# Kernel optimization log

Hardware: AMD Instinct MI355X
Metric: run time of the kernel (lower is better)

Reference implementation:

```python
import jax, jax.numpy as jnp
import numpy as np

PATCH = 16
EPS = 1e-5


def _conv_offsets(x, offset_w, offset_b):
    # offset conv: same kernel/stride/padding as the deform conv
    off = jax.lax.conv_general_dilated(
        x, offset_w, window_strides=(PATCH, PATCH), padding='VALID',
        dimension_numbers=('NCHW', 'OIHW', 'NCHW'))
    return off + offset_b[None, :, None, None]


def _deform_conv(x, offset_w, offset_b, dconv_w):
    B, C, H, W = x.shape
    kh = kw = PATCH
    K = kh * kw
    Ho, Wo = H // PATCH, W // PATCH

    off = _conv_offsets(x, offset_w, offset_b)            # [B, 2K, Ho, Wo]
    # mmcv layout: channels are (dy, dx) pairs per kernel point
    off = off.reshape(B, K, 2, Ho, Wo)
    dy = off[:, :, 0].transpose(0, 2, 3, 1)               # [B, Ho, Wo, K]
    dx = off[:, :, 1].transpose(0, 2, 3, 1)

    ii, jj = jnp.meshgrid(jnp.arange(kh), jnp.arange(kw), indexing='ij')
    ki = ii.reshape(-1).astype(x.dtype)                   # [K]
    kj = jj.reshape(-1).astype(x.dtype)
    base_y = (jnp.arange(Ho, dtype=x.dtype) * PATCH)[:, None] + ki[None, :]  # [Ho, K]
    base_x = (jnp.arange(Wo, dtype=x.dtype) * PATCH)[:, None] + kj[None, :]  # [Wo, K]

    py = base_y[None, :, None, :] + dy                    # [B, Ho, Wo, K]
    px = base_x[None, None, :, :] + dx

    y0 = jnp.floor(py); x0 = jnp.floor(px)
    wy1 = py - y0; wx1 = px - x0
    wy0 = 1.0 - wy1; wx0 = 1.0 - wx1
    y0i = y0.astype(jnp.int32); x0i = x0.astype(jnp.int32)
    y1i = y0i + 1;              x1i = x0i + 1

    xt = x.transpose(0, 2, 3, 1)                          # [B, H, W, C]
    bidx = jnp.arange(B)[:, None, None, None]

    def gather(yi, xi):
        ok = ((yi >= 0) & (yi < H) & (xi >= 0) & (xi < W)).astype(x.dtype)
        v = xt[bidx, jnp.clip(yi, 0, H - 1), jnp.clip(xi, 0, W - 1)]  # [B,Ho,Wo,K,C]
        return v * ok[..., None]

    sampled = (gather(y0i, x0i) * (wy0 * wx0)[..., None]
               + gather(y0i, x1i) * (wy0 * wx1)[..., None]
               + gather(y1i, x0i) * (wy1 * wx0)[..., None]
               + gather(y1i, x1i) * (wy1 * wx1)[..., None])  # [B,Ho,Wo,K,C]

    Wk = dconv_w.reshape(dconv_w.shape[0], C, K)          # [O, C, K]
    out = jnp.einsum('bhwkc,ock->bohw', sampled, Wk)      # [B, O, Ho, Wo]
    return out


def setup_inputs() -> dict:
    key = jax.random.key(0)
    ks = jax.random.split(key, 3)
    B, C, H, W = 64, 3, 224, 224
    O = 768
    x = jax.random.normal(ks[0], (B, C, H, W), jnp.float32)
    # small offset weights -> offsets of O(1) pixel, exercising bilinear path
    offset_w = jax.random.normal(ks[1], (2 * PATCH * PATCH, C, PATCH, PATCH), jnp.float32) * 0.01
    offset_b = jnp.zeros((2 * PATCH * PATCH,), jnp.float32)
    dconv_w = jax.random.normal(ks[2], (O, C, PATCH, PATCH), jnp.float32) * 0.02
    bn_gamma = jnp.ones((O,), jnp.float32)
    bn_beta = jnp.zeros((O,), jnp.float32)
    return {"x": x, "offset_w": offset_w, "offset_b": offset_b,
            "dconv_w": dconv_w, "bn_gamma": bn_gamma, "bn_beta": bn_beta}


def reference(x, offset_w, offset_b, dconv_w, bn_gamma, bn_beta):
    B = x.shape[0]
    y = _deform_conv(x, offset_w, offset_b, dconv_w)      # [B, O, Ho, Wo]
    # BatchNorm2d (training-mode batch stats, biased var) per torch semantics
    mean = jnp.mean(y, axis=(0, 2, 3), keepdims=True)
    var = jnp.mean((y - mean) ** 2, axis=(0, 2, 3), keepdims=True)
    yn = (y - mean) * jax.lax.rsqrt(var + EPS)
    yn = yn * bn_gamma[None, :, None, None] + bn_beta[None, :, None, None]
    ya = jax.nn.gelu(yn, approximate=False)               # nn.GELU default = exact
    O, Ho, Wo = ya.shape[1], ya.shape[2], ya.shape[3]
    return ya.reshape(B, O, Ho * Wo).transpose(0, 2, 1)   # [B, N, embed_dim]
```

## Files before the change

### kernel.cpp

```cpp
#include <hip/hip_runtime.h>
#include <math.h>

#define PATCH 16
#define BATCH 64
#define CIN 3
#define HH 224
#define WW 224
#define NPATCH (BATCH*14*14)
#define KDIM 768
#define NOFF 512
#define NOUT 768
#define KPTS 256
#define EPSF 1e-5f
#define CHW (CIN*HH*WW)
#define HWX (HH*WW)
#define NRB (NPATCH/128)

using short8 = __attribute__((ext_vector_type(8))) short;
using f32x4  = __attribute__((ext_vector_type(4))) float;

#define GLOAD16(g, l) __builtin_amdgcn_global_load_lds( \
    (const __attribute__((address_space(1))) void*)(g), \
    (__attribute__((address_space(3))) void*)(l), 16, 0, 0)

__device__ __forceinline__ unsigned short f2bf(float f) {
    unsigned int u = __float_as_uint(f);
    u = (u + 0x7fffu + ((u >> 16) & 1u)) >> 16;
    return (unsigned short)u;
}
__device__ __forceinline__ float bf2f(unsigned short h) {
    return __uint_as_float(((unsigned int)h) << 16);
}
__device__ __forceinline__ float gelu_exact(float v) {
    return 0.5f * v * (1.0f + erff(v * 0.70710678118654752440f));
}

#define N4X (BATCH*CHW/4)
#define N4W1 (NOFF*KDIM/4)
#define N4W2 (NOUT*KDIM/4)
#define N4ALL (N4X+N4W1+N4W2)

__global__ __launch_bounds__(256) void cvt_all(
    const float* __restrict__ x, const float* __restrict__ w1,
    const float* __restrict__ w2, unsigned short* __restrict__ xbf,
    unsigned short* __restrict__ wbf1, unsigned short* __restrict__ wbf2)
{
    for (int i = blockIdx.x*256 + threadIdx.x; i < N4ALL; i += gridDim.x*256) {
        const float* src; unsigned short* dst; int j;
        if (i < N4X)            { src = x;  dst = xbf;  j = i; }
        else if (i < N4X+N4W1)  { src = w1; dst = wbf1; j = i - N4X; }
        else                    { src = w2; dst = wbf2; j = i - N4X - N4W1; }
        float4 v = ((const float4*)src)[j];
        ((ushort4*)dst)[j] = make_ushort4(f2bf(v.x), f2bf(v.y), f2bf(v.z), f2bf(v.w));
    }
}

__global__ __launch_bounds__(256) void gemm_offsets(
    const unsigned short* __restrict__ xbf, const unsigned short* __restrict__ Bw,
    const float* __restrict__ offb, unsigned short* __restrict__ off)
{
    __shared__ unsigned short lds[4*8192];
    const int t = threadIdx.x;
    const int lane = t & 63;
    const int w = t >> 6, wr = w >> 1, wc = w & 1;

    int bid = blockIdx.x;
    int idx = (bid & 7)*49 + (bid >> 3);
    const int bm = (idx >> 2) * 128, bn = (idx & 3) * 128;

    const int rq = t >> 2;
    const int ksw = (((t & 3) ^ ((t >> 3) & 3)) << 3);

    const unsigned short* aBase0;
    const unsigned short* aBase1;
    {
        int p0 = bm + rq,      b0 = p0/196, r0 = p0%196;
        int p1 = bm + 64 + rq, b1 = p1/196, r1 = p1%196;
        aBase0 = xbf + (size_t)b0*CHW + (size_t)((r0/14)*PATCH)*WW + (size_t)((r0%14)*PATCH);
        aBase1 = xbf + (size_t)b1*CHW + (size_t)((r1/14)*PATCH)*WW + (size_t)((r1%14)*PATCH);
    }
    const unsigned short* bS0 = Bw + (size_t)(bn + rq)*KDIM + ksw;
    const unsigned short* bS1 = Bw + (size_t)(bn + 64 + rq)*KDIM + ksw;

    const int row_a = wr*64 + (lane & 15);
    const int row_b = wc*64 + (lane & 15);
    const int klocs = (((lane >> 4) ^ ((lane >> 1) & 3)) << 3);

#define STG1(slot, k0) do { \
        unsigned short* d = lds + (slot)*8192 + t*8; \
        int e = (k0) + ksw; \
        size_t xo = (size_t)(e >> 8)*HWX + (size_t)((e >> 4) & 15)*WW + (e & 15); \
        GLOAD16(aBase0 + xo, d); \
        GLOAD16(aBase1 + xo, d + 2048); \
        GLOAD16(bS0 + (k0), d + 4096); \
        GLOAD16(bS1 + (k0), d + 6144); \
    } while(0)

    f32x4 acc[4][4] = {};
    STG1(0, 0); STG1(1, 32); STG1(2, 64);
    asm volatile("s_waitcnt vmcnt(8)" ::: "memory");
    __builtin_amdgcn_s_barrier();
#pragma unroll
    for (int it = 0; it < 24; ++it) {
        if (it + 3 < 24) STG1((it+3)&3, (it+3)*32);
        const unsigned short* As_ = lds + (it&3)*8192;
        const unsigned short* Bs_ = As_ + 4096;
        short8 af[4], bv[4];
#pragma unroll
        for (int m = 0; m < 4; ++m) af[m] = *(const short8*)&As_[(row_a + m*16)*32 + klocs];
#pragma unroll
        for (int n = 0; n < 4; ++n) bv[n] = *(const short8*)&Bs_[(row_b + n*16)*32 + klocs];
        __builtin_amdgcn_s_setprio(1);
#pragma unroll
        for (int m = 0; m < 4; ++m)
#pragma unroll
            for (int n = 0; n < 4; ++n)
                acc[m][n] = __builtin_amdgcn_mfma_f32_16x16x32_bf16(af[m], bv[n], acc[m][n], 0, 0, 0);
        __builtin_amdgcn_s_setprio(0);
        if (it <= 20)      { asm volatile("s_waitcnt vmcnt(8) lgkmcnt(0)" ::: "memory"); __builtin_amdgcn_s_barrier(); }
        else if (it == 21) { asm volatile("s_waitcnt vmcnt(4) lgkmcnt(0)" ::: "memory"); __builtin_amdgcn_s_barrier(); }
        else if (it == 22) { asm volatile("s_waitcnt vmcnt(0) lgkmcnt(0)" ::: "memory"); __builtin_amdgcn_s_barrier(); }
    }
#undef STG1

    const int col0 = bn + wc*64 + (lane & 15);
    const int r0 = (lane >> 4) * 4;
#pragma unroll
    for (int m = 0; m < 4; ++m) {
        int grow = bm + wr*64 + m*16 + r0;
#pragma unroll
        for (int n = 0; n < 4; ++n) {
            int gcol = col0 + n*16;
            float bias = offb[gcol];
#pragma unroll
            for (int r = 0; r < 4; ++r)
                off[(size_t)(grow + r)*NOFF + gcol] = f2bf(acc[m][n][r] + bias);
        }
    }
}

__global__ __launch_bounds__(256) void sampler(
    const unsigned short* __restrict__ xbf, const unsigned int* __restrict__ offu,
    unsigned short* __restrict__ A2)
{
    __shared__ unsigned short win[3][22][24];
    int p = blockIdx.x;
    int k = threadIdx.x;
    int b = p / 196, rem = p % 196;
    int ho = rem / 14, wo = rem % 14;
    const int gy0 = ho*PATCH - 2, gx0 = wo*PATCH - 2;
    const unsigned short* xb = xbf + (size_t)b*CHW;

    bool interior = (ho >= 1) && (ho <= 12) && (wo >= 1) && (wo <= 12);
    if (interior) {
        for (int idx = k; idx < 3*22*11; idx += 256) {
            int c = idx / 242, r2 = idx - c*242;
            int row = r2 / 11, u = r2 - row*11;
            const unsigned int* src = (const unsigned int*)
                (xb + (size_t)c*HWX + (size_t)(gy0+row)*WW + gx0);
            *(unsigned int*)&win[c][row][2*u] = src[u];
        }
    } else {
        for (int idx = k; idx < 3*22*22; idx += 256) {
            int c = idx / 484, r2 = idx - c*484;
            int row = r2 / 22, col = r2 - row*22;
            int gy = min(max(gy0+row, 0), HH-1);
            int gx = min(max(gx0+col, 0), WW-1);
            win[c][row][col] = xb[(size_t)c*HWX + (size_t)gy*WW + gx];
        }
    }
    __syncthreads();

    unsigned int d2 = offu[(size_t)p*KPTS + k];
    float dy = __uint_as_float((d2 & 0xffffu) << 16);
    float dx = __uint_as_float(d2 & 0xffff0000u);
    float py = (float)(ho*PATCH + (k >> 4)) + dy;
    float px = (float)(wo*PATCH + (k & 15)) + dx;
    float fy = floorf(py), fx = floorf(px);
    float wy1 = py - fy, wx1 = px - fx;
    float wy0 = 1.f - wy1, wx0 = 1.f - wx1;
    int y0 = (int)fy, x0 = (int)fx;
    int y1 = y0 + 1, x1 = x0 + 1;
    bool oky0 = (y0 >= 0) & (y0 < HH);
    bool oky1 = (y1 >= 0) & (y1 < HH);
    bool okx0 = (x0 >= 0) & (x0 < WW);
    bool okx1 = (x1 >= 0) & (x1 < WW);
    float w00 = wy0*wx0, w01 = wy0*wx1, w10 = wy1*wx0, w11 = wy1*wx1;

    int ry = y0 - gy0, rx = x0 - gx0;
    if (ry >= 0 && ry <= 20 && rx >= 0 && rx <= 20) {
        float m00 = oky0 && okx0 ? 1.f : 0.f;
        float m01 = oky0 && okx1 ? 1.f : 0.f;
        float m10 = oky1 && okx0 ? 1.f : 0.f;
        float m11 = oky1 && okx1 ? 1.f : 0.f;
#pragma unroll
        for (int c = 0; c < CIN; ++c) {
            float v00 = bf2f(win[c][ry  ][rx  ]) * m00;
            float v01 = bf2f(win[c][ry  ][rx+1]) * m01;
            float v10 = bf2f(win[c][ry+1][rx  ]) * m10;
            float v11 = bf2f(win[c][ry+1][rx+1]) * m11;
            float v = v00*w00 + v01*w01 + v10*w10 + v11*w11;
            A2[(size_t)p*KDIM + c*KPTS + k] = f2bf(v);
        }
    } else {
        int yc0 = min(max(y0, 0), HH-1), yc1 = min(max(y1, 0), HH-1);
        int xc0 = min(max(x0, 0), WW-1), xc1 = min(max(x1, 0), WW-1);
#pragma unroll
        for (int c = 0; c < CIN; ++c) {
            const unsigned short* xc = xb + (size_t)c*HWX;
            float v00 = (oky0 && okx0) ? bf2f(xc[(size_t)yc0*WW + xc0]) : 0.f;
            float v01 = (oky0 && okx1) ? bf2f(xc[(size_t)yc0*WW + xc1]) : 0.f;
            float v10 = (oky1 && okx0) ? bf2f(xc[(size_t)yc1*WW + xc0]) : 0.f;
            float v11 = (oky1 && okx1) ? bf2f(xc[(size_t)yc1*WW + xc1]) : 0.f;
            float v = v00*w00 + v01*w01 + v10*w10 + v11*w11;
            A2[(size_t)p*KDIM + c*KPTS + k] = f2bf(v);
        }
    }
}

__global__ __launch_bounds__(512) void gemm_deform(
    const unsigned short* __restrict__ A, const unsigned short* __restrict__ Bw,
    unsigned short* __restrict__ Cbf, float* __restrict__ psum, float* __restrict__ psq)
{
    __shared__ unsigned short lds[4*16384];
    const int t = threadIdx.x;
    const int lane = t & 63;
    const int w = t >> 6;
    const int wr = w >> 2, wc = w & 3;

    int bid = blockIdx.x;
    int xcd = bid & 7, jj = bid >> 3;
    int idx = (xcd < 3) ? xcd*19 + jj : 57 + (xcd-3)*18 + jj;
    const int mblk = idx / 3;
    const int bm = mblk*256, bn = (idx % 3)*256;

    const int schunk = ((t & 3) ^ ((t >> 3) & 3)) << 3;
    const unsigned short* aSrc = A  + (size_t)(bm + (t >> 2))*KDIM + schunk;
    const unsigned short* bSrc = Bw + (size_t)(bn + (t >> 2))*KDIM + schunk;

#define STG_A(s, k0) do { \
        unsigned short* d = lds + (s)*16384 + t*8; \
        GLOAD16(aSrc + (k0), d); \
        GLOAD16(aSrc + (size_t)128*KDIM + (k0), d + 4096); } while(0)
#define STG_B(s, k0) do { \
        unsigned short* d = lds + (s)*16384 + 8192 + t*8; \
        GLOAD16(bSrc + (k0), d); \
        GLOAD16(bSrc + (size_t)128*KDIM + (k0), d + 4096); } while(0)

    const int klocs = (((lane >> 4) ^ ((lane >> 1) & 3)) << 3);
    const int arow0 = wr*128 + (lane & 15);
    const int brow0 = wc*64  + (lane & 15);

    f32x4 acc[8][4] = {};

    STG_A(0, 0);  STG_B(0, 0);
    STG_A(1, 32); STG_B(1, 32);
    asm volatile("s_waitcnt vmcnt(4)" ::: "memory");
    __builtin_amdgcn_s_barrier();

    short8 af[8], bv[4];
    for (int kt = 0; kt < 12; ++kt) {
        const int s0 = (2*kt) & 3;
        const int s1 = s0 + 1;
        const int s2 = (s0 + 2) & 3;
        const int s3 = (s0 + 3) & 3;
        const int k2 = (2*kt + 2) * 32;
        const int k3 = (2*kt + 3) * 32;
        const unsigned short* H0 = lds + s0*16384;
        const unsigned short* H1 = lds + s1*16384;

#pragma unroll
        for (int m = 0; m < 8; ++m) af[m] = *(const short8*)&H0[(arow0 + m*16)*32 + klocs];
        bv[0] = *(const short8*)&H0[8192 + (brow0 +  0)*32 + klocs];
        bv[1] = *(const short8*)&H0[8192 + (brow0 + 16)*32 + klocs];
        if (kt < 11) STG_A(s2, k2);
        __builtin_amdgcn_s_barrier();
        asm volatile("s_waitcnt lgkmcnt(0)" ::: "memory");
        __builtin_amdgcn_s_setprio(1);
#pragma unroll
        for (int m = 0; m < 8; ++m) {
            acc[m][0] = __builtin_amdgcn_mfma_f32_16x16x32_bf16(af[m], bv[0], acc[m][0], 0, 0, 0);
            acc[m][1] = __builtin_amdgcn_mfma_f32_16x16x32_bf16(af[m], bv[1], acc[m][1], 0, 0, 0);
        }
        __builtin_amdgcn_s_setprio(0);
        asm volatile("s_waitcnt lgkmcnt(0)" ::: "memory");
        __builtin_amdgcn_s_barrier();

        bv[2] = *(const short8*)&H0[8192 + (brow0 + 32)*32 + klocs];
        bv[3] = *(const short8*)&H0[8192 + (brow0 + 48)*32 + klocs];
        if (kt < 11) { STG_B(s2, k2);
            asm volatile("s_waitcnt vmcnt(4)" ::: "memory");
        } else {
            asm volatile("s_waitcnt vmcnt(0)" ::: "memory");
        }
        __builtin_amdgcn_s_barrier();
        asm volatile("s_waitcnt lgkmcnt(0)" ::: "memory");
        __builtin_amdgcn_s_setprio(1);
#pragma unroll
        for (int m = 0; m < 8; ++m) {
            acc[m][2] = __builtin_amdgcn_mfma_f32_16x16x32_bf16(af[m], bv[2], acc[m][2], 0, 0, 0);
            acc[m][3] = __builtin_amdgcn_mfma_f32_16x16x32_bf16(af[m], bv[3], acc[m][3], 0, 0, 0);
        }
        __builtin_amdgcn_s_setprio(0);
        asm volatile("s_waitcnt lgkmcnt(0)" ::: "memory");
        __builtin_amdgcn_s_barrier();

#pragma unroll
        for (int m = 0; m < 8; ++m) af[m] = *(const short8*)&H1[(arow0 + m*16)*32 + klocs];
        bv[0] = *(const short8*)&H1[8192 + (brow0 +  0)*32 + klocs];
        bv[1] = *(const short8*)&H1[8192 + (brow0 + 16)*32 + klocs];
        if (kt < 11) STG_A(s3, k3);
        __builtin_amdgcn_s_barrier();
        asm volatile("s_waitcnt lgkmcnt(0)" ::: "memory");
        __builtin_amdgcn_s_setprio(1);
#pragma unroll
        for (int m = 0; m < 8; ++m) {
            acc[m][0] = __builtin_amdgcn_mfma_f32_16x16x32_bf16(af[m], bv[0], acc[m][0], 0, 0, 0);
            acc[m][1] = __builtin_amdgcn_mfma_f32_16x16x32_bf16(af[m], bv[1], acc[m][1], 0, 0, 0);
        }
        __builtin_amdgcn_s_setprio(0);
        asm volatile("s_waitcnt lgkmcnt(0)" ::: "memory");
        __builtin_amdgcn_s_barrier();

        bv[2] = *(const short8*)&H1[8192 + (brow0 + 32)*32 + klocs];
        bv[3] = *(const short8*)&H1[8192 + (brow0 + 48)*32 + klocs];
        if (kt < 11) { STG_B(s3, k3);
            asm volatile("s_waitcnt vmcnt(4)" ::: "memory");
        }
        __builtin_amdgcn_s_barrier();
        asm volatile("s_waitcnt lgkmcnt(0)" ::: "memory");
        __builtin_amdgcn_s_setprio(1);
#pragma unroll
        for (int m = 0; m < 8; ++m) {
            acc[m][2] = __builtin_amdgcn_mfma_f32_16x16x32_bf16(af[m], bv[2], acc[m][2], 0, 0, 0);
            acc[m][3] = __builtin_amdgcn_mfma_f32_16x16x32_bf16(af[m], bv[3], acc[m][3], 0, 0, 0);
        }
        __builtin_amdgcn_s_setprio(0);
        asm volatile("s_waitcnt lgkmcnt(0)" ::: "memory");
        __builtin_amdgcn_s_barrier();
    }
#undef STG_A
#undef STG_B

    float s[4] = {}, q[4] = {};
#pragma unroll
    for (int m = 0; m < 8; ++m)
#pragma unroll
        for (int n = 0; n < 4; ++n)
#pragma unroll
            for (int r = 0; r < 4; ++r) {
                float v = acc[m][n][r];
                s[n] += v; q[n] += v*v;
            }
#pragma unroll
    for (int n = 0; n < 4; ++n) {
        s[n] += __shfl_xor(s[n], 16); q[n] += __shfl_xor(q[n], 16);
        s[n] += __shfl_xor(s[n], 32); q[n] += __shfl_xor(q[n], 32);
    }

    __syncthreads();
    float* redS = (float*)lds;
    float* redQ = redS + 512;
    if (lane < 16) {
#pragma unroll
        for (int n = 0; n < 4; ++n) {
            redS[wr*256 + wc*64 + n*16 + lane] = s[n];
            redQ[wr*256 + wc*64 + n*16 + lane] = q[n];
        }
    }
    __syncthreads();

    const int col0 = bn + wc*64 + (lane & 15);
    const int r0 = (lane >> 4) * 4;
#pragma unroll
    for (int m = 0; m < 8; ++m) {
        int grow = bm + wr*128 + m*16 + r0;
#pragma unroll
        for (int n = 0; n < 4; ++n) {
            int gcol = col0 + n*16;
#pragma unroll
            for (int r = 0; r < 4; ++r)
                Cbf[(size_t)(grow + r)*NOUT + gcol] = f2bf(acc[m][n][r]);
        }
    }
    {
        int half = t >> 8;
        int c = t & 255;
        psum[(size_t)(bm/128 + half)*NOUT + bn + c] = redS[half*256 + c];
        psq [(size_t)(bm/128 + half)*NOUT + bn + c] = redQ[half*256 + c];
    }
}

__global__ __launch_bounds__(256) void bn_final(
    const float* __restrict__ psum, const float* __restrict__ psq,
    const float* __restrict__ gamma, const float* __restrict__ beta,
    float* __restrict__ scale, float* __restrict__ shift)
{
    int o = blockIdx.x*256 + threadIdx.x;
    float s = 0.f, q = 0.f;
    for (int i = 0; i < NRB; ++i) {
        s += psum[(size_t)i*NOUT + o];
        q += psq [(size_t)i*NOUT + o];
    }
    float mean = s * (1.0f/(float)NPATCH);
    float var  = q * (1.0f/(float)NPATCH) - mean*mean;
    float inv  = 1.0f / sqrtf(var + EPSF);
    float sc   = gamma[o] * inv;
    scale[o] = sc;
    shift[o] = beta[o] - mean*sc;
}

__global__ __launch_bounds__(256) void norm_gelu(
    const unsigned short* __restrict__ ybf, float* __restrict__ out,
    const float* __restrict__ scale, const float* __restrict__ shift)
{
    __shared__ float ssc[NOUT], ssh[NOUT];
    for (int i = threadIdx.x; i < NOUT; i += 256) { ssc[i] = scale[i]; ssh[i] = shift[i]; }
    __syncthreads();
    const size_t total8 = (size_t)NPATCH * NOUT / 8;
    for (size_t i = (size_t)blockIdx.x*256 + threadIdx.x; i < total8;
         i += (size_t)gridDim.x*256) {
        uint4 v = ((const uint4*)ybf)[i];
        int og = (int)(i % (NOUT/8)) * 8;
        float4 o0, o1;
        o0.x = gelu_exact(__uint_as_float(v.x << 16)        * ssc[og+0] + ssh[og+0]);
        o0.y = gelu_exact(__uint_as_float(v.x & 0xffff0000u)* ssc[og+1] + ssh[og+1]);
        o0.z = gelu_exact(__uint_as_float(v.y << 16)        * ssc[og+2] + ssh[og+2]);
        o0.w = gelu_exact(__uint_as_float(v.y & 0xffff0000u)* ssc[og+3] + ssh[og+3]);
        o1.x = gelu_exact(__uint_as_float(v.z << 16)        * ssc[og+4] + ssh[og+4]);
        o1.y = gelu_exact(__uint_as_float(v.z & 0xffff0000u)* ssc[og+5] + ssh[og+5]);
        o1.z = gelu_exact(__uint_as_float(v.w << 16)        * ssc[og+6] + ssh[og+6]);
        o1.w = gelu_exact(__uint_as_float(v.w & 0xffff0000u)* ssc[og+7] + ssh[og+7]);
        ((float4*)out)[2*i]   = o0;
        ((float4*)out)[2*i+1] = o1;
    }
}

extern "C" void kernel_launch(void* const* d_in, const int* in_sizes, int n_in,
                              void* d_out, int out_size, void* d_ws, size_t ws_size,
                              hipStream_t stream)
{
    const float* x      = (const float*)d_in[0];
    const float* offw   = (const float*)d_in[1];
    const float* offb   = (const float*)d_in[2];
    const float* dconvw = (const float*)d_in[3];
    const float* gamma  = (const float*)d_in[4];
    const float* beta   = (const float*)d_in[5];
    float* out = (float*)d_out;

    const size_t NX  = (size_t)BATCH*CHW;
    const size_t NW1 = (size_t)NOFF*KDIM;
    const size_t NW2 = (size_t)NOUT*KDIM;

    unsigned short* xbf   = (unsigned short*)d_ws;
    unsigned short* wbf1  = xbf  + NX;
    unsigned short* wbf2  = wbf1 + NW1;
    unsigned short* A2    = wbf2 + NW2;
    unsigned short* off   = A2   + (size_t)NPATCH*KDIM;
    unsigned short* ybf   = off  + (size_t)NPATCH*NOFF;
    float* fscratch = (float*)(ybf + (size_t)NPATCH*NOUT);
    float* psum  = fscratch;
    float* psq   = psum + NRB*NOUT;
    float* scale = psq  + NRB*NOUT;
    float* shift = scale + NOUT;

    cvt_all<<<4096, 256, 0, stream>>>(x, offw, dconvw, xbf, wbf1, wbf2);
    gemm_offsets<<<392, 256, 0, stream>>>(xbf, wbf1, offb, off);
    sampler<<<NPATCH, 256, 0, stream>>>(xbf, (const unsigned int*)off, A2);
    gemm_deform<<<147, 512, 0, stream>>>(A2, wbf2, ybf, psum, psq);
    bn_final<<<3, 256, 0, stream>>>(psum, psq, gamma, beta, scale, shift);
    norm_gelu<<<2048, 256, 0, stream>>>(ybf, out, scale, shift);
}
```

Baseline: 102.7 us.

## Drop separate bf16 conversion of input; read fp32 x directly in GEMM and sampler

Removes the bf16 conversion pass over the input image. The offset GEMM now stages fp32 patches into LDS and packs them to bf16 in registers before the MFMA, and the sampler reads fp32 directly. The conversion kernel now only handles the weights. This saves a full read and write of x, at the cost of more LDS per stage (pipeline depth cut from 4 to 3 slots), twice the A-tile global traffic, and truncating rather than rounding the GEMM's A operand to bf16.

Result: slower. 107.5 us (+4.7%).

```diff
diff --git a/kernel.cpp b/kernel.cpp
--- a/kernel.cpp
+++ b/kernel.cpp
@@ -28,38 +28,35 @@
     u = (u + 0x7fffu + ((u >> 16) & 1u)) >> 16;
     return (unsigned short)u;
 }
-__device__ __forceinline__ float bf2f(unsigned short h) {
-    return __uint_as_float(((unsigned int)h) << 16);
-}
 __device__ __forceinline__ float gelu_exact(float v) {
     return 0.5f * v * (1.0f + erff(v * 0.70710678118654752440f));
 }
-
-#define N4X (BATCH*CHW/4)
+__device__ __forceinline__ unsigned int pk2(float lo, float hi) {
+    return (__float_as_uint(hi) & 0xffff0000u) | (__float_as_uint(lo) >> 16);
+}
+
 #define N4W1 (NOFF*KDIM/4)
 #define N4W2 (NOUT*KDIM/4)
-#define N4ALL (N4X+N4W1+N4W2)
-
-__global__ __launch_bounds__(256) void cvt_all(
-    const float* __restrict__ x, const float* __restrict__ w1,
-    const float* __restrict__ w2, unsigned short* __restrict__ xbf,
+#define N4W  (N4W1+N4W2)
+
+__global__ __launch_bounds__(256) void cvt_w(
+    const float* __restrict__ w1, const float* __restrict__ w2,
     unsigned short* __restrict__ wbf1, unsigned short* __restrict__ wbf2)
 {
-    for (int i = blockIdx.x*256 + threadIdx.x; i < N4ALL; i += gridDim.x*256) {
-        const float* src; unsigned short* dst; int j;
-        if (i < N4X)            { src = x;  dst = xbf;  j = i; }
-        else if (i < N4X+N4W1)  { src = w1; dst = wbf1; j = i - N4X; }
-        else                    { src = w2; dst = wbf2; j = i - N4X - N4W1; }
-        float4 v = ((const float4*)src)[j];
-        ((ushort4*)dst)[j] = make_ushort4(f2bf(v.x), f2bf(v.y), f2bf(v.z), f2bf(v.w));
-    }
+    int i = blockIdx.x*256 + threadIdx.x;
+    if (i >= N4W) return;
+    const float* src; unsigned short* dst; int j;
+    if (i < N4W1) { src = w1; dst = wbf1; j = i; }
+    else          { src = w2; dst = wbf2; j = i - N4W1; }
+    float4 v = ((const float4*)src)[j];
+    ((ushort4*)dst)[j] = make_ushort4(f2bf(v.x), f2bf(v.y), f2bf(v.z), f2bf(v.w));
 }
 
 __global__ __launch_bounds__(256) void gemm_offsets(
-    const unsigned short* __restrict__ xbf, const unsigned short* __restrict__ Bw,
+    const float* __restrict__ x, const unsigned short* __restrict__ Bw,
     const float* __restrict__ offb, unsigned short* __restrict__ off)
 {
-    __shared__ unsigned short lds[4*8192];
+    __shared__ unsigned short lds[3*12288];
     const int t = threadIdx.x;
     const int lane = t & 63;
     const int w = t >> 6, wr = w >> 1, wc = w & 1;
@@ -68,48 +65,60 @@
     int idx = (bid & 7)*49 + (bid >> 3);
     const int bm = (idx >> 2) * 128, bn = (idx & 3) * 128;
 
+    const int sccA = (t & 7) ^ ((t >> 3) & 7);
+    const float* aBase[4];
+#pragma unroll
+    for (int o = 0; o < 4; ++o) {
+        int p = bm + o*32 + (t >> 3);
+        int b = p / 196, rem = p % 196;
+        int ho = rem / 14, wo = rem % 14;
+        aBase[o] = x + (size_t)b*CHW + (size_t)(ho*PATCH)*WW + (size_t)(wo*PATCH);
+    }
     const int rq = t >> 2;
-    const int ksw = (((t & 3) ^ ((t >> 3) & 3)) << 3);
-
-    const unsigned short* aBase0;
-    const unsigned short* aBase1;
-    {
-        int p0 = bm + rq,      b0 = p0/196, r0 = p0%196;
-        int p1 = bm + 64 + rq, b1 = p1/196, r1 = p1%196;
-        aBase0 = xbf + (size_t)b0*CHW + (size_t)((r0/14)*PATCH)*WW + (size_t)((r0%14)*PATCH);
-        aBase1 = xbf + (size_t)b1*CHW + (size_t)((r1/14)*PATCH)*WW + (size_t)((r1%14)*PATCH);
-    }
-    const unsigned short* bS0 = Bw + (size_t)(bn + rq)*KDIM + ksw;
-    const unsigned short* bS1 = Bw + (size_t)(bn + 64 + rq)*KDIM + ksw;
+    const int kswB = (((t & 3) ^ ((t >> 3) & 3)) << 3);
+    const unsigned short* bS0 = Bw + (size_t)(bn + rq)*KDIM + kswB;
+    const unsigned short* bS1 = Bw + (size_t)(bn + 64 + rq)*KDIM + kswB;
 
     const int row_a = wr*64 + (lane & 15);
     const int row_b = wc*64 + (lane & 15);
-    const int klocs = (((lane >> 4) ^ ((lane >> 1) & 3)) << 3);
+    const int cA0 = ((lane >> 4) << 1) ^ (lane & 7);
+    const int klocsB = (((lane >> 4) ^ ((lane >> 1) & 3)) << 3);
 
 #define STG1(slot, k0) do { \
-        unsigned short* d = lds + (slot)*8192 + t*8; \
-        int e = (k0) + ksw; \
+        unsigned short* dA = lds + (slot)*12288 + t*8; \
+        int e = (k0) + sccA*4; \
         size_t xo = (size_t)(e >> 8)*HWX + (size_t)((e >> 4) & 15)*WW + (e & 15); \
-        GLOAD16(aBase0 + xo, d); \
-        GLOAD16(aBase1 + xo, d + 2048); \
-        GLOAD16(bS0 + (k0), d + 4096); \
-        GLOAD16(bS1 + (k0), d + 6144); \
+        GLOAD16(aBase[0] + xo, dA); \
+        GLOAD16(aBase[1] + xo, dA + 2048); \
+        GLOAD16(aBase[2] + xo, dA + 4096); \
+        GLOAD16(aBase[3] + xo, dA + 6144); \
+        unsigned short* dB = lds + (slot)*12288 + 8192 + t*8; \
+        GLOAD16(bS0 + (k0), dB); \
+        GLOAD16(bS1 + (k0), dB + 2048); \
     } while(0)
 
     f32x4 acc[4][4] = {};
-    STG1(0, 0); STG1(1, 32); STG1(2, 64);
-    asm volatile("s_waitcnt vmcnt(8)" ::: "memory");
+    STG1(0, 0); STG1(1, 32);
+    asm volatile("s_waitcnt vmcnt(6)" ::: "memory");
     __builtin_amdgcn_s_barrier();
 #pragma unroll
     for (int it = 0; it < 24; ++it) {
-        if (it + 3 < 24) STG1((it+3)&3, (it+3)*32);
-        const unsigned short* As_ = lds + (it&3)*8192;
-        const unsigned short* Bs_ = As_ + 4096;
+        if (it + 2 < 24) STG1((it+2)%3, (it+2)*32);
+        const float* Af = (const float*)(lds + (it%3)*12288);
+        const unsigned short* Bs_ = lds + (it%3)*12288 + 8192;
         short8 af[4], bv[4];
 #pragma unroll
-        for (int m = 0; m < 4; ++m) af[m] = *(const short8*)&As_[(row_a + m*16)*32 + klocs];
-#pragma unroll
-        for (int n = 0; n < 4; ++n) bv[n] = *(const short8*)&Bs_[(row_b + n*16)*32 + klocs];
+        for (int m = 0; m < 4; ++m) {
+            int rb = (row_a + m*16)*32;
+            f32x4 v0 = *(const f32x4*)&Af[rb + cA0*4];
+            f32x4 v1 = *(const f32x4*)&Af[rb + (cA0^1)*4];
+            uint4 u;
+            u.x = pk2(v0[0], v0[1]); u.y = pk2(v0[2], v0[3]);
+            u.z = pk2(v1[0], v1[1]); u.w = pk2(v1[2], v1[3]);
+            af[m] = *(short8*)&u;
+        }
+#pragma unroll
+        for (int n = 0; n < 4; ++n) bv[n] = *(const short8*)&Bs_[(row_b + n*16)*32 + klocsB];
         __builtin_amdgcn_s_setprio(1);
 #pragma unroll
         for (int m = 0; m < 4; ++m)
@@ -117,8 +126,7 @@
             for (int n = 0; n < 4; ++n)
                 acc[m][n] = __builtin_amdgcn_mfma_f32_16x16x32_bf16(af[m], bv[n], acc[m][n], 0, 0, 0);
         __builtin_amdgcn_s_setprio(0);
-        if (it <= 20)      { asm volatile("s_waitcnt vmcnt(8) lgkmcnt(0)" ::: "memory"); __builtin_amdgcn_s_barrier(); }
-        else if (it == 21) { asm volatile("s_waitcnt vmcnt(4) lgkmcnt(0)" ::: "memory"); __builtin_amdgcn_s_barrier(); }
+        if (it < 22)       { asm volatile("s_waitcnt vmcnt(6) lgkmcnt(0)" ::: "memory"); __builtin_amdgcn_s_barrier(); }
         else if (it == 22) { asm volatile("s_waitcnt vmcnt(0) lgkmcnt(0)" ::: "memory"); __builtin_amdgcn_s_barrier(); }
     }
 #undef STG1
@@ -140,25 +148,24 @@
 }
 
 __global__ __launch_bounds__(256) void sampler(
-    const unsigned short* __restrict__ xbf, const unsigned int* __restrict__ offu,
+    const float* __restrict__ x, const unsigned int* __restrict__ offu,
     unsigned short* __restrict__ A2)
 {
-    __shared__ unsigned short win[3][22][24];
+    __shared__ float win[3][22][24];
     int p = blockIdx.x;
     int k = threadIdx.x;
     int b = p / 196, rem = p % 196;
     int ho = rem / 14, wo = rem % 14;
     const int gy0 = ho*PATCH - 2, gx0 = wo*PATCH - 2;
-    const unsigned short* xb = xbf + (size_t)b*CHW;
+    const float* xb = x + (size_t)b*CHW;
 
     bool interior = (ho >= 1) && (ho <= 12) && (wo >= 1) && (wo <= 12);
     if (interior) {
         for (int idx = k; idx < 3*22*11; idx += 256) {
             int c = idx / 242, r2 = idx - c*242;
             int row = r2 / 11, u = r2 - row*11;
-            const unsigned int* src = (const unsigned int*)
-                (xb + (size_t)c*HWX + (size_t)(gy0+row)*WW + gx0);
-            *(unsigned int*)&win[c][row][2*u] = src[u];
+            float2 s = *(const float2*)(xb + (size_t)c*HWX + (size_t)(gy0+row)*WW + gx0 + 2*u);
+            *(float2*)&win[c][row][2*u] = s;
         }
     } else {
         for (int idx = k; idx < 3*22*22; idx += 256) {
@@ -195,11 +202,10 @@
         float m11 = oky1 && okx1 ? 1.f : 0.f;
 #pragma unroll
         for (int c = 0; c < CIN; ++c) {
-            float v00 = bf2f(win[c][ry  ][rx  ]) * m00;
-            float v01 = bf2f(win[c][ry  ][rx+1]) * m01;
-            float v10 = bf2f(win[c][ry+1][rx  ]) * m10;
-            float v11 = bf2f(win[c][ry+1][rx+1]) * m11;
-            float v = v00*w00 + v01*w01 + v10*w10 + v11*w11;
+            float v = win[c][ry  ][rx  ] * m00 * w00
+                    + win[c][ry  ][rx+1] * m01 * w01
+                    + win[c][ry+1][rx  ] * m10 * w10
+                    + win[c][ry+1][rx+1] * m11 * w11;
             A2[(size_t)p*KDIM + c*KPTS + k] = f2bf(v);
         }
     } else {
@@ -207,11 +213,11 @@
         int xc0 = min(max(x0, 0), WW-1), xc1 = min(max(x1, 0), WW-1);
 #pragma unroll
         for (int c = 0; c < CIN; ++c) {
-            const unsigned short* xc = xb + (size_t)c*HWX;
-            float v00 = (oky0 && okx0) ? bf2f(xc[(size_t)yc0*WW + xc0]) : 0.f;
-            float v01 = (oky0 && okx1) ? bf2f(xc[(size_t)yc0*WW + xc1]) : 0.f;
-            float v10 = (oky1 && okx0) ? bf2f(xc[(size_t)yc1*WW + xc0]) : 0.f;
-            float v11 = (oky1 && okx1) ? bf2f(xc[(size_t)yc1*WW + xc1]) : 0.f;
+            const float* xc = xb + (size_t)c*HWX;
+            float v00 = (oky0 && okx0) ? xc[(size_t)yc0*WW + xc0] : 0.f;
+            float v01 = (oky0 && okx1) ? xc[(size_t)yc0*WW + xc1] : 0.f;
+            float v10 = (oky1 && okx0) ? xc[(size_t)yc1*WW + xc0] : 0.f;
+            float v11 = (oky1 && okx1) ? xc[(size_t)yc1*WW + xc1] : 0.f;
             float v = v00*w00 + v01*w01 + v10*w10 + v11*w11;
             A2[(size_t)p*KDIM + c*KPTS + k] = f2bf(v);
         }
@@ -448,12 +454,10 @@
     const float* beta   = (const float*)d_in[5];
     float* out = (float*)d_out;
 
-    const size_t NX  = (size_t)BATCH*CHW;
     const size_t NW1 = (size_t)NOFF*KDIM;
     const size_t NW2 = (size_t)NOUT*KDIM;
 
-    unsigned short* xbf   = (unsigned short*)d_ws;
-    unsigned short* wbf1  = xbf  + NX;
+    unsigned short* wbf1  = (unsigned short*)d_ws;
     unsigned short* wbf2  = wbf1 + NW1;
     unsigned short* A2    = wbf2 + NW2;
     unsigned short* off   = A2   + (size_t)NPATCH*KDIM;
@@ -464,9 +468,9 @@
     float* scale = psq  + NRB*NOUT;
     float* shift = scale + NOUT;
 
-    cvt_all<<<4096, 256, 0, stream>>>(x, offw, dconvw, xbf, wbf1, wbf2);
-    gemm_offsets<<<392, 256, 0, stream>>>(xbf, wbf1, offb, off);
-    sampler<<<NPATCH, 256, 0, stream>>>(xbf, (const unsigned int*)off, A2);
+    cvt_w<<<(N4W + 255)/256, 256, 0, stream>>>(offw, dconvw, wbf1, wbf2);
+    gemm_offsets<<<392, 256, 0, stream>>>(x, wbf1, offb, off);
+    sampler<<<NPATCH, 256, 0, stream>>>(x, (const unsigned int*)off, A2);
     gemm_deform<<<147, 512, 0, stream>>>(A2, wbf2, ybf, psum, psq);
     bn_final<<<3, 256, 0, stream>>>(psum, psq, gamma, beta, scale, shift);
     norm_gelu<<<2048, 256, 0, stream>>>(ybf, out, scale, shift);
```
